# Kernel optimization log

Measured on AMD Instinct MI355X. Metric: run time of the kernel, lower is better.

Reference implementation:

```python
import jax, jax.numpy as jnp
import numpy as np

N_HEAD = 10

def setup_inputs() -> dict:
    key = jax.random.key(0)
    k1, k2, k3 = jax.random.split(key, 3)
    n_embd = 640
    x = jax.random.normal(k1, (4, 2048, n_embd), dtype=jnp.float32)
    w_qkv = jax.random.normal(k2, (3 * n_embd, n_embd), dtype=jnp.float32) * (1.0 / np.sqrt(n_embd))
    w_proj = jax.random.normal(k3, (n_embd, n_embd), dtype=jnp.float32) * (1.0 / np.sqrt(n_embd))
    return {"x": x, "w_qkv": w_qkv, "w_proj": w_proj}

def reference(x, w_qkv, w_proj):
    bsz, seqlen, n_embd = x.shape
    head_dim = n_embd // N_HEAD
    qkv = jnp.einsum('bsd,ed->bse', x, w_qkv)  # [B,S,3E]
    q, k, v = jnp.split(qkv, 3, axis=2)
    # [B,H,S,Dh]
    q = q.reshape(bsz, seqlen, N_HEAD, head_dim).transpose(0, 2, 1, 3)
    k = k.reshape(bsz, seqlen, N_HEAD, head_dim).transpose(0, 2, 1, 3)
    v = v.reshape(bsz, seqlen, N_HEAD, head_dim).transpose(0, 2, 1, 3)
    scale = 1.0 / np.sqrt(head_dim).astype(np.float32)
    scores = jnp.einsum('bhqd,bhkd->bhqk', q, k) * scale
    causal = jnp.tril(jnp.ones((seqlen, seqlen), dtype=bool))
    scores = jnp.where(causal, scores, jnp.finfo(scores.dtype).min)
    attn = jax.nn.softmax(scores, axis=-1)
    y = jnp.einsum('bhqk,bhkd->bhqd', attn, v)
    y = y.transpose(0, 2, 1, 3).reshape(bsz, seqlen, n_embd)
    return jnp.einsum('bsd,ed->bse', y, w_proj)
```

## Files before the change

kernel.cpp:

```cpp
#include <hip/hip_runtime.h>

#define BB 4
#define SS 2048
#define EE 640
#define NHH 10
#define DHH 64
#define MTOK 8192
#define E33 1920

#define LDST 72

typedef float f32x4 __attribute__((ext_vector_type(4)));
typedef __bf16 bf16x8 __attribute__((ext_vector_type(8)));
typedef unsigned short u16;
typedef u16 u16x4 __attribute__((ext_vector_type(4)));

__device__ inline u16 f2bf(float f) {
  unsigned u = __builtin_bit_cast(unsigned, f);
  u += 0x7fffu + ((u >> 16) & 1u);
  return (u16)(u >> 16);
}

__global__ void convert_kernel(const float* __restrict__ in, u16* __restrict__ out, int n4) {
  int i = blockIdx.x * blockDim.x + threadIdx.x;
  if (i < n4) {
    float4 v = ((const float4*)in)[i];
    u16x4 o = { f2bf(v.x), f2bf(v.y), f2bf(v.z), f2bf(v.w) };
    ((u16x4*)out)[i] = o;
  }
}

__global__ __launch_bounds__(256) void gemm_qkv(
    const u16* __restrict__ A, const u16* __restrict__ Bt,
    u16* __restrict__ qb, u16* __restrict__ kb, u16* __restrict__ vt) {
  __shared__ __align__(16) u16 As[128 * LDST];
  __shared__ __align__(16) u16 Bs[128 * LDST];
  const int t = threadIdx.x;
  const int m0 = blockIdx.y * 128;
  const int n0 = blockIdx.x * 128;
  const int w = t >> 6, lane = t & 63, n16 = lane & 15, quad = lane >> 4;
  const int wm = w >> 1, wn = w & 1;

  f32x4 acc[4][4];
  for (int i = 0; i < 4; i++)
    for (int j = 0; j < 4; j++) acc[i][j] = f32x4{0.f, 0.f, 0.f, 0.f};

  for (int kt = 0; kt < 10; ++kt) {
    __syncthreads();
    for (int i = 0; i < 4; ++i) {
      int c = i * 256 + t;
      int row = c >> 3, col0 = (c & 7) * 8;
      *(bf16x8*)&As[row * LDST + col0] = *(const bf16x8*)&A[(m0 + row) * 640 + kt * 64 + col0];
      *(bf16x8*)&Bs[row * LDST + col0] = *(const bf16x8*)&Bt[(n0 + row) * 640 + kt * 64 + col0];
    }
    __syncthreads();
    for (int ks = 0; ks < 2; ++ks) {
      bf16x8 a[4], b[4];
      for (int mi = 0; mi < 4; mi++)
        a[mi] = *(const bf16x8*)&As[(wm * 64 + mi * 16 + n16) * LDST + ks * 32 + quad * 8];
      for (int ni = 0; ni < 4; ni++)
        b[ni] = *(const bf16x8*)&Bs[(wn * 64 + ni * 16 + n16) * LDST + ks * 32 + quad * 8];
      for (int mi = 0; mi < 4; mi++)
        for (int ni = 0; ni < 4; ni++)
          acc[mi][ni] = __builtin_amdgcn_mfma_f32_16x16x32_bf16(a[mi], b[ni], acc[mi][ni], 0, 0, 0);
    }
  }

  const int which = n0 / 640;
  for (int ni = 0; ni < 4; ni++) {
    int col = n0 + wn * 64 + ni * 16 + n16;
    int eh = col - which * 640;
    int h = eh >> 6, d = eh & 63;
    for (int mi = 0; mi < 4; mi++) {
      int tb = m0 + wm * 64 + mi * 16 + quad * 4;
      f32x4 c = acc[mi][ni];
      if (which == 2) {
        int b_ = tb >> 11, s_ = tb & 2047;
        u16x4 pk = { f2bf(c[0]), f2bf(c[1]), f2bf(c[2]), f2bf(c[3]) };
        *(u16x4*)&vt[((b_ * NHH + h) * DHH + d) * SS + s_] = pk;
      } else {
        u16* dst = (which == 0) ? qb : kb;
        for (int r = 0; r < 4; r++) {
          int tok = tb + r;
          int b_ = tok >> 11, s_ = tok & 2047;
          dst[((b_ * NHH + h) * SS + s_) * DHH + d] = f2bf(c[r]);
        }
      }
    }
  }
}

__global__ __launch_bounds__(256) void attn_kernel(
    const u16* __restrict__ qb, const u16* __restrict__ kb, const u16* __restrict__ vt,
    u16* __restrict__ y) {
  __shared__ __align__(16) u16 Ks[2][64 * LDST];
  __shared__ __align__(16) u16 Vs[2][64 * LDST];
  const int t = threadIdx.x;
  const int w = t >> 6, lane = t & 63, n16 = lane & 15, quad = lane >> 4;
  const int bh = blockIdx.x;
  const int qt = 31 - blockIdx.y;
  const int qb0 = qt * 64;
  const int b_ = bh / NHH, h = bh % NHH;

  bf16x8 aq[2];
  {
    const u16* qp = &qb[(bh * SS + qb0 + w * 16 + n16) * DHH];
    aq[0] = *(const bf16x8*)&qp[quad * 8];
    aq[1] = *(const bf16x8*)&qp[32 + quad * 8];
  }
  const int q_rel = w * 16 + n16;

  const int c1 = 256 + t;
  const int row0 = t >> 3,  col0 = (t & 7) * 8;
  const int row1 = c1 >> 3, col1 = (c1 & 7) * 8;
  auto perm = [](int k) {
    int p = k >> 5, rem = k & 31, qd = rem >> 3, tt = rem & 7;
    return ((p << 1) | (tt >> 2)) * 16 + qd * 4 + (tt & 3);
  };
  const int prow0 = perm(row0), prow1 = perm(row1);

  float4 fk0, fk1, fv0, fv1;
  fk0 = *(const float4*)&kb[(bh * SS + row0) * DHH + col0];
  fk1 = *(const float4*)&kb[(bh * SS + row1) * DHH + col1];
  fv0 = *(const float4*)&vt[(bh * DHH + row0) * SS + col0];
  fv1 = *(const float4*)&vt[(bh * DHH + row1) * SS + col1];
  *(float4*)&Ks[0][prow0 * LDST + col0] = fk0;
  *(float4*)&Ks[0][prow1 * LDST + col1] = fk1;
  *(float4*)&Vs[0][row0 * LDST + col0] = fv0;
  *(float4*)&Vs[0][row1 * LDST + col1] = fv1;

  float m_i = -1e30f, l_i = 0.f;
  f32x4 o[4];
  for (int db = 0; db < 4; db++) o[db] = f32x4{0.f, 0.f, 0.f, 0.f};

  for (int kt = 0; kt <= qt; ++kt) {
    __syncthreads();
    const int cur = kt & 1, nxt = cur ^ 1;
    if (kt < qt) {
      int kk = (kt + 1) * 64;
      fk0 = *(const float4*)&kb[(bh * SS + kk + row0) * DHH + col0];
      fk1 = *(const float4*)&kb[(bh * SS + kk + row1) * DHH + col1];
      fv0 = *(const float4*)&vt[(bh * DHH + row0) * SS + kk + col0];
      fv1 = *(const float4*)&vt[(bh * DHH + row1) * SS + kk + col1];
    }

    f32x4 sc[4];
    for (int nb = 0; nb < 4; nb++) {
      f32x4 c = f32x4{0.f, 0.f, 0.f, 0.f};
      for (int ks = 0; ks < 2; ks++) {
        bf16x8 ak = *(const bf16x8*)&Ks[cur][(nb * 16 + n16) * LDST + ks * 32 + quad * 8];
        c = __builtin_amdgcn_mfma_f32_16x16x32_bf16(ak, aq[ks], c, 0, 0, 0);
      }
      sc[nb] = c;
    }
    const bool diag = (kt == qt);
    for (int nb = 0; nb < 4; nb++)
      for (int r = 0; r < 4; r++) {
        float v = sc[nb][r] * 0.125f;
        int key = ((nb >> 1) << 5) + quad * 8 + ((nb & 1) << 2) + r;
        sc[nb][r] = (diag && key > q_rel) ? -1e30f : v;
      }

    float rm = -1e30f;
    for (int nb = 0; nb < 4; nb++)
      for (int r = 0; r < 4; r++) rm = fmaxf(rm, sc[nb][r]);
    rm = fmaxf(rm, __shfl_xor(rm, 16));
    rm = fmaxf(rm, __shfl_xor(rm, 32));
    float mnew = fmaxf(m_i, rm);
    float alpha = __expf(m_i - mnew);
    float p[4][4];
    float rs = 0.f;
    for (int nb = 0; nb < 4; nb++)
      for (int r = 0; r < 4; r++) { float pv = __expf(sc[nb][r] - mnew); p[nb][r] = pv; rs += pv; }
    rs += __shfl_xor(rs, 16);
    rs += __shfl_xor(rs, 32);
    l_i = l_i * alpha + rs;
    m_i = mnew;
    for (int db = 0; db < 4; db++)
      for (int r = 0; r < 4; r++) o[db][r] *= alpha;

    for (int p2 = 0; p2 < 2; p2++) {
      union { bf16x8 v; u16 s[8]; } bp;
      for (int j = 0; j < 4; j++) {
        bp.s[j]     = f2bf(p[2 * p2][j]);
        bp.s[4 + j] = f2bf(p[2 * p2 + 1][j]);
      }
      for (int db = 0; db < 4; db++) {
        bf16x8 av = *(const bf16x8*)&Vs[cur][(db * 16 + n16) * LDST + p2 * 32 + quad * 8];
        o[db] = __builtin_amdgcn_mfma_f32_16x16x32_bf16(av, bp.v, o[db], 0, 0, 0);
      }
    }

    if (kt < qt) {
      *(float4*)&Ks[nxt][prow0 * LDST + col0] = fk0;
      *(float4*)&Ks[nxt][prow1 * LDST + col1] = fk1;
      *(float4*)&Vs[nxt][row0 * LDST + col0] = fv0;
      *(float4*)&Vs[nxt][row1 * LDST + col1] = fv1;
    }
  }

  const float inv = 1.0f / l_i;
  const int tok = b_ * SS + qb0 + w * 16 + n16;
  for (int db = 0; db < 4; db++) {
    u16x4 pk = { f2bf(o[db][0] * inv), f2bf(o[db][1] * inv),
                 f2bf(o[db][2] * inv), f2bf(o[db][3] * inv) };
    *(u16x4*)&y[tok * EE + h * DHH + db * 16 + quad * 4] = pk;
  }
}

__global__ __launch_bounds__(256) void gemm_proj(
    const u16* __restrict__ A, const u16* __restrict__ Bt, float* __restrict__ out) {
  __shared__ __align__(16) u16 As[128 * LDST];
  __shared__ __align__(16) u16 Bs[128 * LDST];
  const int t = threadIdx.x;
  const int m0 = blockIdx.y * 128;
  const int n0 = blockIdx.x * 128;
  const int w = t >> 6, lane = t & 63, n16 = lane & 15, quad = lane >> 4;
  const int wm = w >> 1, wn = w & 1;

  f32x4 acc[4][4];
  for (int i = 0; i < 4; i++)
    for (int j = 0; j < 4; j++) acc[i][j] = f32x4{0.f, 0.f, 0.f, 0.f};

  for (int kt = 0; kt < 10; ++kt) {
    __syncthreads();
    for (int i = 0; i < 4; ++i) {
      int c = i * 256 + t;
      int row = c >> 3, col0 = (c & 7) * 8;
      *(bf16x8*)&As[row * LDST + col0] = *(const bf16x8*)&A[(m0 + row) * 640 + kt * 64 + col0];
      *(bf16x8*)&Bs[row * LDST + col0] = *(const bf16x8*)&Bt[(n0 + row) * 640 + kt * 64 + col0];
    }
    __syncthreads();
    for (int ks = 0; ks < 2; ++ks) {
      bf16x8 a[4], b[4];
      for (int mi = 0; mi < 4; mi++)
        a[mi] = *(const bf16x8*)&As[(wm * 64 + mi * 16 + n16) * LDST + ks * 32 + quad * 8];
      for (int ni = 0; ni < 4; ni++)
        b[ni] = *(const bf16x8*)&Bs[(wn * 64 + ni * 16 + n16) * LDST + ks * 32 + quad * 8];
      for (int mi = 0; mi < 4; mi++)
        for (int ni = 0; ni < 4; ni++)
          acc[mi][ni] = __builtin_amdgcn_mfma_f32_16x16x32_bf16(a[mi], b[ni], acc[mi][ni], 0, 0, 0);
    }
  }

  for (int ni = 0; ni < 4; ni++) {
    int col = n0 + wn * 64 + ni * 16 + n16;
    for (int mi = 0; mi < 4; mi++) {
      int rowb = m0 + wm * 64 + mi * 16 + quad * 4;
      f32x4 c = acc[mi][ni];
      for (int r = 0; r < 4; r++) out[(rowb + r) * 640 + col] = c[r];
    }
  }
}

extern "C" void kernel_launch(void* const* d_in, const int* in_sizes, int n_in,
                              void* d_out, int out_size, void* d_ws, size_t ws_size,
                              hipStream_t stream) {
  const float* x     = (const float*)d_in[0];
  const float* wqkv  = (const float*)d_in[1];
  const float* wproj = (const float*)d_in[2];
  float* out = (float*)d_out;

  char* ws = (char*)d_ws;
  u16* xb     = (u16*)(ws + 0);
  u16* wqkvb  = (u16*)(ws + 10485760);
  u16* wprojb = (u16*)(ws + 12943360);
  u16* qbuf   = (u16*)(ws + 13762560);
  u16* kbuf   = (u16*)(ws + 24248320);
  u16* vtb    = (u16*)(ws + 34734080);
  u16* ybuf   = (u16*)(ws + 45219840);

  convert_kernel<<<5120, 256, 0, stream>>>(x, xb, 5242880 / 4);
  convert_kernel<<<1200, 256, 0, stream>>>(wqkv, wqkvb, 1228800 / 4);
  convert_kernel<<<400, 256, 0, stream>>>(wproj, wprojb, 409600 / 4);

  gemm_qkv<<<dim3(15, 64), 256, 0, stream>>>(xb, wqkvb, qbuf, kbuf, vtb);
  attn_kernel<<<dim3(40, 32), 256, 0, stream>>>(qbuf, kbuf, vtb, ybuf);
  gemm_proj<<<dim3(5, 64), 256, 0, stream>>>(ybuf, wprojb, out);
}
```

Measured before the change: 183.4 us.

## Fold softmax scale into Q, use exp2, lazy rescaling, and hardware bf16 casts

Result: faster. 179.8 us (-2.0%).

```diff
diff --git a/kernel.cpp b/kernel.cpp
--- a/kernel.cpp
+++ b/kernel.cpp
@@ -10,8 +10,17 @@
 
 #define LDST 72
 
+#if __has_builtin(__builtin_amdgcn_exp2f)
+#define EXP2(x) __builtin_amdgcn_exp2f(x)
+#else
+#define EXP2(x) exp2f(x)
+#endif
+
+#define QSCALE 0.18033688011112042f
+
 typedef float f32x4 __attribute__((ext_vector_type(4)));
 typedef __bf16 bf16x8 __attribute__((ext_vector_type(8)));
+typedef __bf16 bf16x4 __attribute__((ext_vector_type(4)));
 typedef unsigned short u16;
 typedef u16 u16x4 __attribute__((ext_vector_type(4)));
 
@@ -74,6 +83,9 @@
     for (int mi = 0; mi < 4; mi++) {
       int tb = m0 + wm * 64 + mi * 16 + quad * 4;
       f32x4 c = acc[mi][ni];
+      if (which == 0) {
+        c[0] *= QSCALE; c[1] *= QSCALE; c[2] *= QSCALE; c[3] *= QSCALE;
+      }
       if (which == 2) {
         int b_ = tb >> 11, s_ = tb & 2047;
         u16x4 pk = { f2bf(c[0]), f2bf(c[1]), f2bf(c[2]), f2bf(c[3]) };
@@ -153,41 +165,50 @@
       }
       sc[nb] = c;
     }
-    const bool diag = (kt == qt);
-    for (int nb = 0; nb < 4; nb++)
-      for (int r = 0; r < 4; r++) {
-        float v = sc[nb][r] * 0.125f;
-        int key = ((nb >> 1) << 5) + quad * 8 + ((nb & 1) << 2) + r;
-        sc[nb][r] = (diag && key > q_rel) ? -1e30f : v;
-      }
-
-    float rm = -1e30f;
-    for (int nb = 0; nb < 4; nb++)
-      for (int r = 0; r < 4; r++) rm = fmaxf(rm, sc[nb][r]);
+    if (kt == qt) {
+      for (int nb = 0; nb < 4; nb++)
+        for (int r = 0; r < 4; r++) {
+          int key = ((nb >> 1) << 5) + quad * 8 + ((nb & 1) << 2) + r;
+          if (key > q_rel) sc[nb][r] = -1e30f;
+        }
+    }
+
+    f32x4 mx;
+    for (int r = 0; r < 4; r++)
+      mx[r] = fmaxf(fmaxf(sc[0][r], sc[1][r]), fmaxf(sc[2][r], sc[3][r]));
+    float rm = fmaxf(fmaxf(mx[0], mx[1]), fmaxf(mx[2], mx[3]));
     rm = fmaxf(rm, __shfl_xor(rm, 16));
     rm = fmaxf(rm, __shfl_xor(rm, 32));
-    float mnew = fmaxf(m_i, rm);
-    float alpha = __expf(m_i - mnew);
-    float p[4][4];
-    float rs = 0.f;
+
+    if (!__all(rm - m_i <= 8.0f)) {
+      float mnew = fmaxf(m_i, rm);
+      float alpha = EXP2(m_i - mnew);
+      l_i *= alpha;
+      for (int db = 0; db < 4; db++)
+        for (int r = 0; r < 4; r++) o[db][r] *= alpha;
+      m_i = mnew;
+    }
+
+    f32x4 ps[4];
     for (int nb = 0; nb < 4; nb++)
-      for (int r = 0; r < 4; r++) { float pv = __expf(sc[nb][r] - mnew); p[nb][r] = pv; rs += pv; }
+      for (int r = 0; r < 4; r++) ps[nb][r] = EXP2(sc[nb][r] - m_i);
+    f32x4 sv;
+    for (int r = 0; r < 4; r++)
+      sv[r] = (ps[0][r] + ps[1][r]) + (ps[2][r] + ps[3][r]);
+    float rs = (sv[0] + sv[1]) + (sv[2] + sv[3]);
     rs += __shfl_xor(rs, 16);
     rs += __shfl_xor(rs, 32);
-    l_i = l_i * alpha + rs;
-    m_i = mnew;
-    for (int db = 0; db < 4; db++)
-      for (int r = 0; r < 4; r++) o[db][r] *= alpha;
+    l_i += rs;
 
     for (int p2 = 0; p2 < 2; p2++) {
-      union { bf16x8 v; u16 s[8]; } bp;
+      bf16x8 bp;
       for (int j = 0; j < 4; j++) {
-        bp.s[j]     = f2bf(p[2 * p2][j]);
-        bp.s[4 + j] = f2bf(p[2 * p2 + 1][j]);
+        bp[j]     = (__bf16)ps[2 * p2][j];
+        bp[4 + j] = (__bf16)ps[2 * p2 + 1][j];
       }
       for (int db = 0; db < 4; db++) {
         bf16x8 av = *(const bf16x8*)&Vs[cur][(db * 16 + n16) * LDST + p2 * 32 + quad * 8];
-        o[db] = __builtin_amdgcn_mfma_f32_16x16x32_bf16(av, bp.v, o[db], 0, 0, 0);
+        o[db] = __builtin_amdgcn_mfma_f32_16x16x32_bf16(av, bp, o[db], 0, 0, 0);
       }
     }
 
@@ -202,9 +223,9 @@
   const float inv = 1.0f / l_i;
   const int tok = b_ * SS + qb0 + w * 16 + n16;
   for (int db = 0; db < 4; db++) {
-    u16x4 pk = { f2bf(o[db][0] * inv), f2bf(o[db][1] * inv),
-                 f2bf(o[db][2] * inv), f2bf(o[db][3] * inv) };
-    *(u16x4*)&y[tok * EE + h * DHH + db * 16 + quad * 4] = pk;
+    bf16x4 pk = { (__bf16)(o[db][0] * inv), (__bf16)(o[db][1] * inv),
+                  (__bf16)(o[db][2] * inv), (__bf16)(o[db][3] * inv) };
+    *(bf16x4*)&y[tok * EE + h * DHH + db * 16 + quad * 4] = pk;
   }
 }
 
```
